# Performance work log

Hardware: AMD Instinct MI355X
Metric: run time of the kernel (lower is better)

Reference implementation:

```python
import jax, jax.numpy as jnp
import numpy as np

M_FACTORS = [8, 8, 8, 8]
N_FACTORS = [8, 8, 8, 8]
RANK = 8
E = 8
B = 8
SEQ = 512
M_IN = int(np.prod(M_FACTORS))   # 4096
N_OUT = int(np.prod(N_FACTORS))  # 4096


def setup_inputs() -> dict:
    key = jax.random.key(0)
    k1, k2, k3, k4, k5 = jax.random.split(key, 5)
    X = jax.random.normal(k1, (B, SEQ, M_IN), dtype=jnp.float32)
    gates = jax.random.uniform(k2, (B, E), dtype=jnp.float32)
    # TT cores: [E, r_i, factor, r_{i+1}]; boundary ranks are 1.
    core_first = jax.random.normal(k3, (E, 1, M_FACTORS[0], RANK), dtype=jnp.float32)
    cores_mid = jax.random.normal(k4, (6, E, RANK, 8, RANK), dtype=jnp.float32)
    core_last = jax.random.normal(k5, (E, RANK, N_FACTORS[-1], 1), dtype=jnp.float32)
    return {"X": X, "gates": gates, "core_first": core_first,
            "cores_mid": cores_mid, "core_last": core_last}


def _tt_forward(X, gates, core_first, cores_mid, core_last):
    b, s, _ = X.shape
    # View X as [B, 1, seq, m_k-1, ..., m_0] (m factors reversed), rank dim = 1.
    tt = X.reshape((b, s) + tuple(M_FACTORS[::-1]))[:, None]
    cores = [core_first] + [cores_mid[i] for i in range(cores_mid.shape[0])] + [core_last]
    num_m = len(M_FACTORS)
    # Input-factor contractions: 'b r ... m, b r m p -> b p ...'
    for i in range(num_m):
        merged = jnp.einsum('be,ermp->brmp', gates, cores[i])  # [B, r, m_f, p]
        tt = jnp.einsum('br...m,brmp->bp...', tt, merged)
    # Output-factor expansions: 'b r ..., b r n p -> b p ... n'
    for i in range(len(N_FACTORS)):
        merged = jnp.einsum('be,ernp->brnp', gates, cores[num_m + i])  # [B, r, n_f, p]
        tt = jnp.einsum('br...,brnp->bp...n', tt, merged)
    return tt.reshape(b, s, -1)  # [B, seq, prod(n_factors)]


def reference(X, gates, core_first, cores_mid, core_last):
    return _tt_forward(X, gates, core_first, cores_mid, core_last)
```

## Files before the change

kernel.cpp:

```cpp
#include <hip/hip_runtime.h>
#include <hip/hip_bf16.h>


#define MC_ 16

__global__ __launch_bounds__(256) void k_compose(
    const float* __restrict__ gates,
    const float* __restrict__ core_first,
    const float* __restrict__ cores_mid,
    const float* __restrict__ core_last,
    __hip_bfloat16* __restrict__ Kinb,
    float* __restrict__ Kout)
{
  const int part = blockIdx.x;
  const int b    = blockIdx.y;
  const int t    = threadIdx.x;

  __shared__ float g[8];
  __shared__ float mg[3200];
  __shared__ __align__(16) float A2[512];
  __shared__ __align__(16) float A3[4096];
  __shared__ __align__(16) float C2[512];
  __shared__ __align__(16) float C3[4096];

  if (t < 8) g[t] = gates[b*8 + t];
  __syncthreads();

  for (int idx = t; idx < 3200; idx += 256) {
    float acc = 0.f;
    if (idx < 64) {
      #pragma unroll
      for (int e = 0; e < 8; ++e) acc += g[e] * core_first[e*64 + idx];
    } else if (idx < 3136) {
      const int i = (idx - 64) >> 9;
      const int w = (idx - 64) & 511;
      #pragma unroll
      for (int e = 0; e < 8; ++e) acc += g[e] * cores_mid[(i*8 + e)*512 + w];
    } else {
      const int w = idx - 3136;
      #pragma unroll
      for (int e = 0; e < 8; ++e) acc += g[e] * core_last[e*64 + w];
    }
    mg[idx] = acc;
  }
  __syncthreads();

  const float* mg0 = mg;
  const float* mg1 = mg + 64;
  const float* mg2 = mg + 64 + 512;
  const float* mg3 = mg + 64 + 1024;
  const float* mg4 = mg + 64 + 1536;
  const float* mg5 = mg + 64 + 2048;
  const float* mg6 = mg + 64 + 2560;
  const float* mg7 = mg + 3136;

  for (int idx = t; idx < 1024; idx += 256) {
    if (idx < 512) {
      const int mm = idx >> 3, p2 = idx & 7;
      const int m1 = mm >> 3, m0 = mm & 7;
      float acc = 0.f;
      #pragma unroll
      for (int p1 = 0; p1 < 8; ++p1)
        acc += mg0[m0*8 + p1] * mg1[p1*64 + m1*8 + p2];
      A2[idx] = acc;
    } else {
      const int id = idx - 512;
      const int p6 = id >> 6, n2 = (id >> 3) & 7, n3 = id & 7;
      float acc = 0.f;
      #pragma unroll
      for (int p7 = 0; p7 < 8; ++p7)
        acc += mg6[p6*64 + n2*8 + p7] * mg7[p7*8 + n3];
      C2[id] = acc;
    }
  }
  __syncthreads();

  for (int idx = t; idx < 8192; idx += 256) {
    if (idx < 4096) {
      const int rest = idx >> 3, p3 = idx & 7;
      const int m2 = rest >> 6, mm = rest & 63;
      float acc = 0.f;
      #pragma unroll
      for (int p2 = 0; p2 < 8; ++p2)
        acc += A2[mm*8 + p2] * mg2[p2*64 + m2*8 + p3];
      A3[idx] = acc;
    } else {
      const int id = idx - 4096;
      const int p5 = id >> 9, n1 = (id >> 6) & 7, nn = id & 63;
      float acc = 0.f;
      #pragma unroll
      for (int p6 = 0; p6 < 8; ++p6)
        acc += mg5[p5*64 + n1*8 + p6] * C2[p6*64 + nn];
      C3[id] = acc;
    }
  }
  __syncthreads();

  {
    __hip_bfloat16* kb = Kinb + ((size_t)b*4096 + part*512)*8;
    #pragma unroll
    for (int rr = 0; rr < 2; ++rr) {
      const int r = t*2 + rr;
      #pragma unroll
      for (int p4 = 0; p4 < 8; ++p4) {
        float acc = 0.f;
        #pragma unroll
        for (int p3 = 0; p3 < 8; ++p3)
          acc += A3[r*8 + p3] * mg3[p3*64 + part*8 + p4];
        kb[r*8 + p4] = __float2bfloat16(acc);
      }
    }
    float* ob = Kout + b*32768 + part*512;
    #pragma unroll
    for (int jj = 0; jj < 2; ++jj) {
      const int j = t*2 + jj;
      #pragma unroll
      for (int p4 = 0; p4 < 8; ++p4) {
        float acc = 0.f;
        #pragma unroll
        for (int p5 = 0; p5 < 8; ++p5)
          acc += mg4[p4*64 + part*8 + p5] * C3[p5*512 + j];
        ob[p4*4096 + j] = acc;
      }
    }
  }
}

__device__ __forceinline__ float bfhi(unsigned u) {
  return __uint_as_float(u & 0xffff0000u);
}
__device__ __forceinline__ float bflo(unsigned u) {
  return __uint_as_float(u << 16);
}

__global__ __launch_bounds__(256) void k_vpart(
    const float* __restrict__ X,
    const uint4* __restrict__ Kinb,
    float* __restrict__ Vpart)
{
  const int sg = blockIdx.x;
  const int mc = blockIdx.y;
  const int b  = blockIdx.z;
  const int t  = threadIdx.x;

  const int w = t >> 6;
  const int l = t & 63;
  const int r = l & 15;
  const int q = l >> 4;

  const int row = sg*64 + w*16 + r;
  const float* xr = X + ((size_t)(b*512 + row))*4096 + mc*256 + q*4;
  const uint4* kr = Kinb + (size_t)b*4096 + mc*256 + q*4;

  float acc[8];
  #pragma unroll
  for (int p = 0; p < 8; ++p) acc[p] = 0.f;

  #pragma unroll 4
  for (int j = 0; j < 16; ++j) {
    const float4 x4 = *(const float4*)(xr + j*16);
    const float xv[4] = {x4.x, x4.y, x4.z, x4.w};
    #pragma unroll
    for (int i = 0; i < 4; ++i) {
      const uint4 k8 = kr[j*16 + i];
      const float xi = xv[i];
      acc[0] += xi * bflo(k8.x);  acc[1] += xi * bfhi(k8.x);
      acc[2] += xi * bflo(k8.y);  acc[3] += xi * bfhi(k8.y);
      acc[4] += xi * bflo(k8.z);  acc[5] += xi * bfhi(k8.z);
      acc[6] += xi * bflo(k8.w);  acc[7] += xi * bfhi(k8.w);
    }
  }

  #pragma unroll
  for (int p = 0; p < 8; ++p) {
    acc[p] += __shfl_xor(acc[p], 16, 64);
    acc[p] += __shfl_xor(acc[p], 32, 64);
  }

  if (l < 16) {
    float* vp = Vpart + ((size_t)((b*MC_ + mc)*512) + row)*8;
    *(float4*)(vp)     = make_float4(acc[0], acc[1], acc[2], acc[3]);
    *(float4*)(vp + 4) = make_float4(acc[4], acc[5], acc[6], acc[7]);
  }
}

__global__ __launch_bounds__(256) void k_out(
    const float* __restrict__ Vpart,
    const float* __restrict__ Kout,
    float* __restrict__ Out)
{
  const int nc = blockIdx.x;
  const int sg = blockIdx.y;
  const int b  = blockIdx.z;
  const int t  = threadIdx.x;

  __shared__ __align__(16) float vs[32*8];

  {
    const float* vp = Vpart + ((size_t)b*MC_*512 + sg*32)*8 + t;
    float a = 0.f;
    #pragma unroll
    for (int mc = 0; mc < MC_; ++mc) a += vp[(size_t)mc*512*8];
    vs[t] = a;
  }

  float4 kr[8];
  {
    const float* kb = Kout + b*32768 + nc*1024 + t*4;
    #pragma unroll
    for (int p = 0; p < 8; ++p) kr[p] = *(const float4*)(kb + p*4096);
  }
  __syncthreads();

  float* ob = Out + (size_t)(b*512 + sg*32)*4096 + nc*1024 + t*4;
  for (int s = 0; s < 32; ++s) {
    const float* vv = &vs[s*8];
    float o0 = 0.f, o1 = 0.f, o2 = 0.f, o3 = 0.f;
    #pragma unroll
    for (int p = 0; p < 8; ++p) {
      const float v = vv[p];
      o0 += v * kr[p].x; o1 += v * kr[p].y; o2 += v * kr[p].z; o3 += v * kr[p].w;
    }
    *(float4*)(ob + (size_t)s*4096) = make_float4(o0, o1, o2, o3);
  }
}

extern "C" void kernel_launch(void* const* d_in, const int* in_sizes, int n_in,
                              void* d_out, int out_size, void* d_ws, size_t ws_size,
                              hipStream_t stream) {
  const float* X     = (const float*)d_in[0];
  const float* gates = (const float*)d_in[1];
  const float* cf    = (const float*)d_in[2];
  const float* cm    = (const float*)d_in[3];
  const float* cl    = (const float*)d_in[4];
  float* out = (float*)d_out;

  float* ws = (float*)d_ws;
  float*          Kout  = ws;
  float*          Vpart = ws + 262144;
  __hip_bfloat16* Kinb  = (__hip_bfloat16*)(ws + 262144 + 524288);

  k_compose<<<dim3(8, 8),        256, 0, stream>>>(gates, cf, cm, cl, Kinb, Kout);
  k_vpart <<<dim3(8, MC_, 8),    256, 0, stream>>>(X, (const uint4*)Kinb, Vpart);
  k_out   <<<dim3(4, 16, 8),     256, 0, stream>>>(Vpart, Kout, out);
}
```

Before: 145.4 us.

## Fuse input projection and output expansion into one kernel per row block

Merges the k_vpart and k_out kernels into a single k_main kernel. Each block handles 8 rows over the full 4096 input width, reduces the rank-8 vector in shared memory, and then writes the 4096-wide output directly. This removes the Vpart round trip through global memory, the split-K partial sums and one kernel launch. The grid shrinks to 512 blocks, and each block now does a long serial reduction plus 32 KB of output writes, which may lower parallelism and memory-level overlap.

```diff
diff --git a/kernel.cpp b/kernel.cpp
--- a/kernel.cpp
+++ b/kernel.cpp
@@ -1,8 +1,6 @@
 #include <hip/hip_runtime.h>
 #include <hip/hip_bf16.h>
 
-
-#define MC_ 16
 
 __global__ __launch_bounds__(256) void k_compose(
     const float* __restrict__ gates,
@@ -133,36 +131,38 @@
   return __uint_as_float(u << 16);
 }
 
-__global__ __launch_bounds__(256) void k_vpart(
+__global__ __launch_bounds__(256) void k_main(
     const float* __restrict__ X,
     const uint4* __restrict__ Kinb,
-    float* __restrict__ Vpart)
+    const float* __restrict__ Kout,
+    float* __restrict__ Out)
 {
   const int sg = blockIdx.x;
-  const int mc = blockIdx.y;
-  const int b  = blockIdx.z;
+  const int b  = blockIdx.y;
   const int t  = threadIdx.x;
-
-  const int w = t >> 6;
-  const int l = t & 63;
-  const int r = l & 15;
-  const int q = l >> 4;
-
-  const int row = sg*64 + w*16 + r;
-  const float* xr = X + ((size_t)(b*512 + row))*4096 + mc*256 + q*4;
-  const uint4* kr = Kinb + (size_t)b*4096 + mc*256 + q*4;
+  const int w  = t >> 6;
+  const int l  = t & 63;
+  const int r  = l & 7;
+  const int q  = l >> 3;
+
+  __shared__ float vred[4][64];
+  __shared__ __align__(16) float vsum[64];
+
+  const int row = sg*8 + r;
+  const float* xr = X + ((size_t)(b*512 + row))*4096 + w*1024 + q*4;
+  const uint4* kr = Kinb + (size_t)b*4096 + w*1024 + q*4;
 
   float acc[8];
   #pragma unroll
   for (int p = 0; p < 8; ++p) acc[p] = 0.f;
 
   #pragma unroll 4
-  for (int j = 0; j < 16; ++j) {
-    const float4 x4 = *(const float4*)(xr + j*16);
+  for (int j = 0; j < 32; ++j) {
+    const float4 x4 = *(const float4*)(xr + j*32);
     const float xv[4] = {x4.x, x4.y, x4.z, x4.w};
     #pragma unroll
     for (int i = 0; i < 4; ++i) {
-      const uint4 k8 = kr[j*16 + i];
+      const uint4 k8 = kr[j*32 + i];
       const float xi = xv[i];
       acc[0] += xi * bflo(k8.x);  acc[1] += xi * bfhi(k8.x);
       acc[2] += xi * bflo(k8.y);  acc[3] += xi * bfhi(k8.y);
@@ -173,55 +173,45 @@
 
   #pragma unroll
   for (int p = 0; p < 8; ++p) {
+    acc[p] += __shfl_xor(acc[p], 8, 64);
     acc[p] += __shfl_xor(acc[p], 16, 64);
     acc[p] += __shfl_xor(acc[p], 32, 64);
   }
-
-  if (l < 16) {
-    float* vp = Vpart + ((size_t)((b*MC_ + mc)*512) + row)*8;
-    *(float4*)(vp)     = make_float4(acc[0], acc[1], acc[2], acc[3]);
-    *(float4*)(vp + 4) = make_float4(acc[4], acc[5], acc[6], acc[7]);
-  }
-}
-
-__global__ __launch_bounds__(256) void k_out(
-    const float* __restrict__ Vpart,
-    const float* __restrict__ Kout,
-    float* __restrict__ Out)
-{
-  const int nc = blockIdx.x;
-  const int sg = blockIdx.y;
-  const int b  = blockIdx.z;
-  const int t  = threadIdx.x;
-
-  __shared__ __align__(16) float vs[32*8];
-
-  {
-    const float* vp = Vpart + ((size_t)b*MC_*512 + sg*32)*8 + t;
-    float a = 0.f;
-    #pragma unroll
-    for (int mc = 0; mc < MC_; ++mc) a += vp[(size_t)mc*512*8];
-    vs[t] = a;
-  }
-
-  float4 kr[8];
-  {
-    const float* kb = Kout + b*32768 + nc*1024 + t*4;
-    #pragma unroll
-    for (int p = 0; p < 8; ++p) kr[p] = *(const float4*)(kb + p*4096);
-  }
-  __syncthreads();
-
-  float* ob = Out + (size_t)(b*512 + sg*32)*4096 + nc*1024 + t*4;
-  for (int s = 0; s < 32; ++s) {
-    const float* vv = &vs[s*8];
-    float o0 = 0.f, o1 = 0.f, o2 = 0.f, o3 = 0.f;
-    #pragma unroll
-    for (int p = 0; p < 8; ++p) {
-      const float v = vv[p];
-      o0 += v * kr[p].x; o1 += v * kr[p].y; o2 += v * kr[p].z; o3 += v * kr[p].w;
-    }
-    *(float4*)(ob + (size_t)s*4096) = make_float4(o0, o1, o2, o3);
+  if (l < 8) {
+    #pragma unroll
+    for (int p = 0; p < 8; ++p) vred[w][l*8 + p] = acc[p];
+  }
+  __syncthreads();
+  if (t < 64) vsum[t] = vred[0][t] + vred[1][t] + vred[2][t] + vred[3][t];
+  __syncthreads();
+
+  float4 va[8], vb[8];
+  #pragma unroll
+  for (int s = 0; s < 8; ++s) {
+    va[s] = *(const float4*)&vsum[s*8];
+    vb[s] = *(const float4*)&vsum[s*8 + 4];
+  }
+
+  const float* kb = Kout + b*32768 + t*4;
+  float* ob = Out + ((size_t)(b*512 + sg*8))*4096 + t*4;
+
+  #pragma unroll
+  for (int nc = 0; nc < 4; ++nc) {
+    float4 kc[8];
+    #pragma unroll
+    for (int p = 0; p < 8; ++p) kc[p] = *(const float4*)(kb + nc*1024 + p*4096);
+    #pragma unroll
+    for (int s = 0; s < 8; ++s) {
+      float o0 = va[s].x*kc[0].x + va[s].y*kc[1].x + va[s].z*kc[2].x + va[s].w*kc[3].x
+               + vb[s].x*kc[4].x + vb[s].y*kc[5].x + vb[s].z*kc[6].x + vb[s].w*kc[7].x;
+      float o1 = va[s].x*kc[0].y + va[s].y*kc[1].y + va[s].z*kc[2].y + va[s].w*kc[3].y
+               + vb[s].x*kc[4].y + vb[s].y*kc[5].y + vb[s].z*kc[6].y + vb[s].w*kc[7].y;
+      float o2 = va[s].x*kc[0].z + va[s].y*kc[1].z + va[s].z*kc[2].z + va[s].w*kc[3].z
+               + vb[s].x*kc[4].z + vb[s].y*kc[5].z + vb[s].z*kc[6].z + vb[s].w*kc[7].z;
+      float o3 = va[s].x*kc[0].w + va[s].y*kc[1].w + va[s].z*kc[2].w + va[s].w*kc[3].w
+               + vb[s].x*kc[4].w + vb[s].y*kc[5].w + vb[s].z*kc[6].w + vb[s].w*kc[7].w;
+      *(float4*)(ob + (size_t)s*4096 + nc*1024) = make_float4(o0, o1, o2, o3);
+    }
   }
 }
 
@@ -236,11 +226,9 @@
   float* out = (float*)d_out;
 
   float* ws = (float*)d_ws;
-  float*          Kout  = ws;
-  float*          Vpart = ws + 262144;
-  __hip_bfloat16* Kinb  = (__hip_bfloat16*)(ws + 262144 + 524288);
-
-  k_compose<<<dim3(8, 8),        256, 0, stream>>>(gates, cf, cm, cl, Kinb, Kout);
-  k_vpart <<<dim3(8, MC_, 8),    256, 0, stream>>>(X, (const uint4*)Kinb, Vpart);
-  k_out   <<<dim3(4, 16, 8),     256, 0, stream>>>(Vpart, Kout, out);
-}
+  float*          Kout = ws;
+  __hip_bfloat16* Kinb = (__hip_bfloat16*)(ws + 262144);
+
+  k_compose<<<dim3(8, 8),   256, 0, stream>>>(gates, cf, cm, cl, Kinb, Kout);
+  k_main   <<<dim3(64, 8),  256, 0, stream>>>(X, (const uint4*)Kinb, Kout, out);
+}
```

Result: no change. 145.8 us (+0.3%).
